# Performance work log

Measured on AMD Instinct MI355X. Metric: run time of the kernel, lower is better.

## Reference

```python
import jax, jax.numpy as jnp
import numpy as np

L, B, I, H, O = 8, 1, 2048, 2048, 1000  # num_layers, batch, input, hidden, output


def setup_inputs() -> dict:
    key = jax.random.key(0)
    ks = jax.random.split(key, 20)
    s = 1.0 / np.sqrt(H)  # torch nn.Linear default init bound

    def w(k, shape):
        return jax.random.uniform(k, shape, jnp.float32, -s, s)

    inp = {
        "x": jax.random.normal(ks[0], (B, 1, I), jnp.float32),
        "h": jax.random.normal(ks[1], (L, B, H), jnp.float32),
    }
    # six gate linears per layer; input_size == hidden_size so all stack to [L, H, H]
    for i, n in enumerate(["W_ir", "W_hr", "W_h1", "W_x1", "W_iu", "W_hu"]):
        inp[n] = w(ks[2 + 2 * i], (L, H, H))
        inp["b" + n[1:]] = w(ks[3 + 2 * i], (L, H))
    inp["W_fc"] = w(ks[14], (O, H))
    inp["b_fc"] = w(ks[15], (O,))
    return inp


def reference(x, h, W_ir, b_ir, W_hr, b_hr, W_h1, b_h1, W_x1, b_x1,
              W_iu, b_iu, W_hu, b_hu, W_fc, b_fc):
    # Layer 0 input is x[:, 0, :]; layer l>0 input is the ORIGINAL h[l-1]
    # (not the freshly computed hidden), so all layers are independent -> batch them.
    inp = jnp.concatenate([x[:, 0, :][None, :, :], h[:-1]], axis=0)  # [L, B, H]

    def lin(v, W, b):  # per-layer torch Linear: v @ W.T + b, batched over L
        return jnp.einsum('lbi,lhi->lbh', v, W) + b[:, None, :]

    reset_gate = jax.nn.sigmoid(lin(inp, W_ir, b_ir) + lin(h, W_hr, b_hr))
    r = jnp.tanh(reset_gate * lin(h, W_h1, b_h1) + lin(inp, W_x1, b_x1))
    update_gate = jax.nn.sigmoid(lin(inp, W_iu, b_iu) + lin(h, W_hu, b_hu))
    new_h = (1.0 - update_gate) * r + update_gate * h  # [L, B, H]

    out = jax.nn.log_softmax(jnp.maximum(new_h[-1], 0.0) @ W_fc.T + b_fc, axis=1)
    return (out, new_h)
```

## Files before the change

### kernel.cpp

```cpp
#include <hip/hip_runtime.h>
#include <math.h>

#define NL 8
#define NH 2048
#define NO 1000

__device__ __forceinline__ float dot4(float4 a, float4 b) {
    return a.x * b.x + a.y * b.y + a.z * b.z + a.w * b.w;
}

__device__ __forceinline__ float4 relu4(float4 a) {
    return make_float4(fmaxf(a.x, 0.f), fmaxf(a.y, 0.f), fmaxf(a.z, 0.f), fmaxf(a.w, 0.f));
}

__device__ __forceinline__ float wave_sum(float v) {
#pragma unroll
    for (int off = 32; off > 0; off >>= 1) v += __shfl_xor(v, off);
    return v;
}

__global__ __launch_bounds__(384) void gru_gates_kernel(
    const float* __restrict__ x,
    const float* __restrict__ h,
    const float* __restrict__ W_ir, const float* __restrict__ b_ir,
    const float* __restrict__ W_hr, const float* __restrict__ b_hr,
    const float* __restrict__ W_h1, const float* __restrict__ b_h1,
    const float* __restrict__ W_x1, const float* __restrict__ b_x1,
    const float* __restrict__ W_iu, const float* __restrict__ b_iu,
    const float* __restrict__ W_hu, const float* __restrict__ b_hu,
    float* __restrict__ new_h)
{
    const int bi   = blockIdx.x;
    const int l    = bi >> 11;
    const int g    = threadIdx.x >> 6;
    const int lane = threadIdx.x & 63;

    __shared__ float part[6];

    const float* __restrict__ W;
    const float* __restrict__ bv;
    const float* vecf;
    const float* vi = (l == 0) ? x : (h + (size_t)(l - 1) * NH);
    const float* vh = h + (size_t)l * NH;
    switch (g) {
        case 0:  W = W_ir; bv = b_ir; vecf = vi; break;
        case 1:  W = W_hr; bv = b_hr; vecf = vh; break;
        case 2:  W = W_h1; bv = b_h1; vecf = vh; break;
        case 3:  W = W_x1; bv = b_x1; vecf = vi; break;
        case 4:  W = W_iu; bv = b_iu; vecf = vi; break;
        default: W = W_hu; bv = b_hu; vecf = vh; break;
    }
    const float4* __restrict__ wrow = (const float4*)(W + (size_t)bi * NH);
    const float4* __restrict__ vec  = (const float4*)vecf;

    const float4 w0 = wrow[lane +   0];
    const float4 w1 = wrow[lane +  64];
    const float4 w2 = wrow[lane + 128];
    const float4 w3 = wrow[lane + 192];
    const float4 w4 = wrow[lane + 256];
    const float4 w5 = wrow[lane + 320];
    const float4 w6 = wrow[lane + 384];
    const float4 w7 = wrow[lane + 448];

    float s;
    s  = dot4(vec[lane +   0], w0);
    s += dot4(vec[lane +  64], w1);
    s += dot4(vec[lane + 128], w2);
    s += dot4(vec[lane + 192], w3);
    s += dot4(vec[lane + 256], w4);
    s += dot4(vec[lane + 320], w5);
    s += dot4(vec[lane + 384], w6);
    s += dot4(vec[lane + 448], w7);

    s = wave_sum(s);
    if (lane == 0) part[g] = s + bv[bi];
    __syncthreads();

    if (threadIdx.x == 0) {
        const float reset = 1.f / (1.f + expf(-(part[0] + part[1])));
        const float r     = tanhf(reset * part[2] + part[3]);
        const float u     = 1.f / (1.f + expf(-(part[4] + part[5])));
        const float hv    = h[bi];
        new_h[bi] = (1.f - u) * r + u * hv;
    }
}

__global__ __launch_bounds__(256) void fc_kernel(
    const float* __restrict__ new_h,
    const float* __restrict__ W_fc,
    const float* __restrict__ b_fc,
    float* __restrict__ logits)
{
    const int wave = (blockIdx.x * blockDim.x + threadIdx.x) >> 6;
    const int lane = threadIdx.x & 63;
    if (wave >= NO) return;
    const float4* __restrict__ v = (const float4*)(new_h + (size_t)(NL - 1) * NH);
    const float4* __restrict__ w = (const float4*)(W_fc + (size_t)wave * NH);
    float s = 0.f;
#pragma unroll
    for (int it = 0; it < NH / 4 / 64 / 2; ++it) {
        const int k0 = it * 128 + lane;
        const int k1 = k0 + 64;
        const float4 v0 = v[k0];
        const float4 w0 = w[k0];
        const float4 v1 = v[k1];
        const float4 w1 = w[k1];
        s += dot4(relu4(v0), w0) + dot4(relu4(v1), w1);
    }
    s = wave_sum(s);
    if (lane == 0) logits[wave] = s + b_fc[wave];
}

__global__ __launch_bounds__(1024) void lsm_kernel(
    const float* __restrict__ logits, float* __restrict__ out)
{
    const int t = threadIdx.x;
    const int lane = t & 63;
    const int wid = t >> 6;
    __shared__ float sred[16];

    const float v = (t < NO) ? logits[t] : -INFINITY;

    float m = v;
#pragma unroll
    for (int off = 32; off > 0; off >>= 1) m = fmaxf(m, __shfl_xor(m, off));
    if (lane == 0) sred[wid] = m;
    __syncthreads();
    if (wid == 0) {
        float mm = (t < 16) ? sred[t] : -INFINITY;
#pragma unroll
        for (int off = 8; off > 0; off >>= 1) mm = fmaxf(mm, __shfl_xor(mm, off));
        if (t == 0) sred[0] = mm;
    }
    __syncthreads();
    const float M = sred[0];
    __syncthreads();

    float e = (t < NO) ? expf(v - M) : 0.f;
    float s = e;
#pragma unroll
    for (int off = 32; off > 0; off >>= 1) s += __shfl_xor(s, off);
    if (lane == 0) sred[wid] = s;
    __syncthreads();
    if (wid == 0) {
        float ss = (t < 16) ? sred[t] : 0.f;
#pragma unroll
        for (int off = 8; off > 0; off >>= 1) ss += __shfl_xor(ss, off);
        if (t == 0) sred[0] = ss;
    }
    __syncthreads();
    const float lse = M + logf(sred[0]);

    if (t < NO) out[t] = v - lse;
}

extern "C" void kernel_launch(void* const* d_in, const int* in_sizes, int n_in,
                              void* d_out, int out_size, void* d_ws, size_t ws_size,
                              hipStream_t stream) {
    const float* x    = (const float*)d_in[0];
    const float* h    = (const float*)d_in[1];
    const float* W_ir = (const float*)d_in[2];
    const float* b_ir = (const float*)d_in[3];
    const float* W_hr = (const float*)d_in[4];
    const float* b_hr = (const float*)d_in[5];
    const float* W_h1 = (const float*)d_in[6];
    const float* b_h1 = (const float*)d_in[7];
    const float* W_x1 = (const float*)d_in[8];
    const float* b_x1 = (const float*)d_in[9];
    const float* W_iu = (const float*)d_in[10];
    const float* b_iu = (const float*)d_in[11];
    const float* W_hu = (const float*)d_in[12];
    const float* b_hu = (const float*)d_in[13];
    const float* W_fc = (const float*)d_in[14];
    const float* b_fc = (const float*)d_in[15];

    float* out    = (float*)d_out;
    float* new_h  = out + NO;
    float* logits = (float*)d_ws;

    gru_gates_kernel<<<NL * NH, 384, 0, stream>>>(
        x, h, W_ir, b_ir, W_hr, b_hr, W_h1, b_h1, W_x1, b_x1,
        W_iu, b_iu, W_hu, b_hu, new_h);

    fc_kernel<<<(NO + 3) / 4, 256, 0, stream>>>(new_h, W_fc, b_fc, logits);

    lsm_kernel<<<1, 1024, 0, stream>>>(logits, out);
}
```

Before: 141.4 us.

## Process four rows per GRU block and fuse FC with log-softmax via last-block counter

The gate kernel now has each block handle four consecutive output rows, so each wave loads its input vector once and reuses it across four weight rows. This cuts the block count fourfold and amortizes vector loads and the block-level sync. The FC and log-softmax kernels are merged: a global atomic counter picks the last finishing block, which then computes the log-softmax over all logits, removing one kernel launch. The price is an extra memset launch, per-block atomics and fences, and higher register pressure in the gate kernel.

```diff
diff --git a/kernel.cpp b/kernel.cpp
--- a/kernel.cpp
+++ b/kernel.cpp
@@ -4,13 +4,10 @@
 #define NL 8
 #define NH 2048
 #define NO 1000
+#define ROWS 4
 
 __device__ __forceinline__ float dot4(float4 a, float4 b) {
     return a.x * b.x + a.y * b.y + a.z * b.z + a.w * b.w;
-}
-
-__device__ __forceinline__ float4 relu4(float4 a) {
-    return make_float4(fmaxf(a.x, 0.f), fmaxf(a.y, 0.f), fmaxf(a.z, 0.f), fmaxf(a.w, 0.f));
 }
 
 __device__ __forceinline__ float wave_sum(float v) {
@@ -30,18 +27,18 @@
     const float* __restrict__ W_hu, const float* __restrict__ b_hu,
     float* __restrict__ new_h)
 {
-    const int bi   = blockIdx.x;
-    const int l    = bi >> 11;
+    const int row0 = blockIdx.x * ROWS;
+    const int l    = row0 >> 11;
     const int g    = threadIdx.x >> 6;
     const int lane = threadIdx.x & 63;
 
-    __shared__ float part[6];
-
+    __shared__ float part[ROWS][6];
+
+    const float* vi = (l == 0) ? x : (h + (size_t)(l - 1) * NH);
+    const float* vh = h + (size_t)l * NH;
     const float* __restrict__ W;
     const float* __restrict__ bv;
     const float* vecf;
-    const float* vi = (l == 0) ? x : (h + (size_t)(l - 1) * NH);
-    const float* vh = h + (size_t)l * NH;
     switch (g) {
         case 0:  W = W_ir; bv = b_ir; vecf = vi; break;
         case 1:  W = W_hr; bv = b_hr; vecf = vh; break;
@@ -50,108 +47,147 @@
         case 4:  W = W_iu; bv = b_iu; vecf = vi; break;
         default: W = W_hu; bv = b_hu; vecf = vh; break;
     }
-    const float4* __restrict__ wrow = (const float4*)(W + (size_t)bi * NH);
-    const float4* __restrict__ vec  = (const float4*)vecf;
-
-    const float4 w0 = wrow[lane +   0];
-    const float4 w1 = wrow[lane +  64];
-    const float4 w2 = wrow[lane + 128];
-    const float4 w3 = wrow[lane + 192];
-    const float4 w4 = wrow[lane + 256];
-    const float4 w5 = wrow[lane + 320];
-    const float4 w6 = wrow[lane + 384];
-    const float4 w7 = wrow[lane + 448];
-
-    float s;
-    s  = dot4(vec[lane +   0], w0);
-    s += dot4(vec[lane +  64], w1);
-    s += dot4(vec[lane + 128], w2);
-    s += dot4(vec[lane + 192], w3);
-    s += dot4(vec[lane + 256], w4);
-    s += dot4(vec[lane + 320], w5);
-    s += dot4(vec[lane + 384], w6);
-    s += dot4(vec[lane + 448], w7);
-
-    s = wave_sum(s);
-    if (lane == 0) part[g] = s + bv[bi];
-    __syncthreads();
-
-    if (threadIdx.x == 0) {
-        const float reset = 1.f / (1.f + expf(-(part[0] + part[1])));
-        const float r     = tanhf(reset * part[2] + part[3]);
-        const float u     = 1.f / (1.f + expf(-(part[4] + part[5])));
-        const float hv    = h[bi];
-        new_h[bi] = (1.f - u) * r + u * hv;
-    }
-}
-
-__global__ __launch_bounds__(256) void fc_kernel(
+    const float4* __restrict__ vec = (const float4*)vecf;
+
+    const float4 v0 = vec[lane +   0];
+    const float4 v1 = vec[lane +  64];
+    const float4 v2 = vec[lane + 128];
+    const float4 v3 = vec[lane + 192];
+    const float4 v4 = vec[lane + 256];
+    const float4 v5 = vec[lane + 320];
+    const float4 v6 = vec[lane + 384];
+    const float4 v7 = vec[lane + 448];
+
+    const float4* __restrict__ wrow = (const float4*)(W + (size_t)row0 * NH);
+
+    float s0, s1, s2, s3;
+    {
+        const float4* __restrict__ wr = wrow;
+        const float4 w0 = wr[lane +   0], w1 = wr[lane +  64];
+        const float4 w2 = wr[lane + 128], w3 = wr[lane + 192];
+        const float4 w4 = wr[lane + 256], w5 = wr[lane + 320];
+        const float4 w6 = wr[lane + 384], w7 = wr[lane + 448];
+        s0 = dot4(v0,w0)+dot4(v1,w1)+dot4(v2,w2)+dot4(v3,w3)
+           + dot4(v4,w4)+dot4(v5,w5)+dot4(v6,w6)+dot4(v7,w7);
+    }
+    {
+        const float4* __restrict__ wr = wrow + (NH / 4);
+        const float4 w0 = wr[lane +   0], w1 = wr[lane +  64];
+        const float4 w2 = wr[lane + 128], w3 = wr[lane + 192];
+        const float4 w4 = wr[lane + 256], w5 = wr[lane + 320];
+        const float4 w6 = wr[lane + 384], w7 = wr[lane + 448];
+        s1 = dot4(v0,w0)+dot4(v1,w1)+dot4(v2,w2)+dot4(v3,w3)
+           + dot4(v4,w4)+dot4(v5,w5)+dot4(v6,w6)+dot4(v7,w7);
+    }
+    {
+        const float4* __restrict__ wr = wrow + 2 * (NH / 4);
+        const float4 w0 = wr[lane +   0], w1 = wr[lane +  64];
+        const float4 w2 = wr[lane + 128], w3 = wr[lane + 192];
+        const float4 w4 = wr[lane + 256], w5 = wr[lane + 320];
+        const float4 w6 = wr[lane + 384], w7 = wr[lane + 448];
+        s2 = dot4(v0,w0)+dot4(v1,w1)+dot4(v2,w2)+dot4(v3,w3)
+           + dot4(v4,w4)+dot4(v5,w5)+dot4(v6,w6)+dot4(v7,w7);
+    }
+    {
+        const float4* __restrict__ wr = wrow + 3 * (NH / 4);
+        const float4 w0 = wr[lane +   0], w1 = wr[lane +  64];
+        const float4 w2 = wr[lane + 128], w3 = wr[lane + 192];
+        const float4 w4 = wr[lane + 256], w5 = wr[lane + 320];
+        const float4 w6 = wr[lane + 384], w7 = wr[lane + 448];
+        s3 = dot4(v0,w0)+dot4(v1,w1)+dot4(v2,w2)+dot4(v3,w3)
+           + dot4(v4,w4)+dot4(v5,w5)+dot4(v6,w6)+dot4(v7,w7);
+    }
+
+    s0 = wave_sum(s0);
+    s1 = wave_sum(s1);
+    s2 = wave_sum(s2);
+    s3 = wave_sum(s3);
+    if (lane == 0) {
+        part[0][g] = s0 + bv[row0 + 0];
+        part[1][g] = s1 + bv[row0 + 1];
+        part[2][g] = s2 + bv[row0 + 2];
+        part[3][g] = s3 + bv[row0 + 3];
+    }
+    __syncthreads();
+
+    if (threadIdx.x < ROWS) {
+        const int r  = threadIdx.x;
+        const int bi = row0 + r;
+        const float reset = 1.f / (1.f + expf(-(part[r][0] + part[r][1])));
+        const float rr    = tanhf(reset * part[r][2] + part[r][3]);
+        const float u     = 1.f / (1.f + expf(-(part[r][4] + part[r][5])));
+        new_h[bi] = (1.f - u) * rr + u * h[bi];
+    }
+}
+
+__global__ __launch_bounds__(256) void fc_lsm_kernel(
     const float* __restrict__ new_h,
     const float* __restrict__ W_fc,
     const float* __restrict__ b_fc,
-    float* __restrict__ logits)
+    float* __restrict__ logits,
+    unsigned int* __restrict__ counter,
+    float* __restrict__ out)
 {
-    const int wave = (blockIdx.x * blockDim.x + threadIdx.x) >> 6;
     const int lane = threadIdx.x & 63;
-    if (wave >= NO) return;
-    const float4* __restrict__ v = (const float4*)(new_h + (size_t)(NL - 1) * NH);
-    const float4* __restrict__ w = (const float4*)(W_fc + (size_t)wave * NH);
-    float s = 0.f;
-#pragma unroll
-    for (int it = 0; it < NH / 4 / 64 / 2; ++it) {
-        const int k0 = it * 128 + lane;
-        const int k1 = k0 + 64;
-        const float4 v0 = v[k0];
-        const float4 w0 = w[k0];
-        const float4 v1 = v[k1];
-        const float4 w1 = w[k1];
-        s += dot4(relu4(v0), w0) + dot4(relu4(v1), w1);
-    }
-    s = wave_sum(s);
-    if (lane == 0) logits[wave] = s + b_fc[wave];
-}
-
-__global__ __launch_bounds__(1024) void lsm_kernel(
-    const float* __restrict__ logits, float* __restrict__ out)
-{
+    const int wid  = threadIdx.x >> 6;
+    const int row  = blockIdx.x * 4 + wid;
+
+    if (row < NO) {
+        const float4* __restrict__ v  = (const float4*)(new_h + (size_t)(NL - 1) * NH);
+        const float4* __restrict__ wt = (const float4*)(W_fc + (size_t)row * NH);
+        float s = 0.f;
+#pragma unroll
+        for (int c = 0; c < 8; ++c) {
+            const int k = c * 64 + lane;
+            float4 vv = v[k];
+            vv.x = fmaxf(vv.x, 0.f); vv.y = fmaxf(vv.y, 0.f);
+            vv.z = fmaxf(vv.z, 0.f); vv.w = fmaxf(vv.w, 0.f);
+            s += dot4(vv, wt[k]);
+        }
+        s = wave_sum(s);
+        if (lane == 0) logits[row] = s + b_fc[row];
+    }
+    __threadfence();
+    __syncthreads();
+
+    __shared__ unsigned int lastflag;
+    if (threadIdx.x == 0)
+        lastflag = (atomicAdd(counter, 1u) == gridDim.x - 1) ? 1u : 0u;
+    __syncthreads();
+    if (!lastflag) return;
+    __threadfence();
+
     const int t = threadIdx.x;
-    const int lane = t & 63;
-    const int wid = t >> 6;
-    __shared__ float sred[16];
-
-    const float v = (t < NO) ? logits[t] : -INFINITY;
-
-    float m = v;
+    float l0 = -INFINITY, l1 = -INFINITY, l2 = -INFINITY, l3 = -INFINITY;
+    if (t       < NO) l0 = logits[t];
+    if (t + 256 < NO) l1 = logits[t + 256];
+    if (t + 512 < NO) l2 = logits[t + 512];
+    if (t + 768 < NO) l3 = logits[t + 768];
+
+    __shared__ float redm[4];
+    float m = fmaxf(fmaxf(l0, l1), fmaxf(l2, l3));
 #pragma unroll
     for (int off = 32; off > 0; off >>= 1) m = fmaxf(m, __shfl_xor(m, off));
-    if (lane == 0) sred[wid] = m;
-    __syncthreads();
-    if (wid == 0) {
-        float mm = (t < 16) ? sred[t] : -INFINITY;
-#pragma unroll
-        for (int off = 8; off > 0; off >>= 1) mm = fmaxf(mm, __shfl_xor(mm, off));
-        if (t == 0) sred[0] = mm;
-    }
-    __syncthreads();
-    const float M = sred[0];
-    __syncthreads();
-
-    float e = (t < NO) ? expf(v - M) : 0.f;
-    float s = e;
-#pragma unroll
-    for (int off = 32; off > 0; off >>= 1) s += __shfl_xor(s, off);
-    if (lane == 0) sred[wid] = s;
-    __syncthreads();
-    if (wid == 0) {
-        float ss = (t < 16) ? sred[t] : 0.f;
-#pragma unroll
-        for (int off = 8; off > 0; off >>= 1) ss += __shfl_xor(ss, off);
-        if (t == 0) sred[0] = ss;
-    }
-    __syncthreads();
-    const float lse = M + logf(sred[0]);
-
-    if (t < NO) out[t] = v - lse;
+    if (lane == 0) redm[wid] = m;
+    __syncthreads();
+    m = fmaxf(fmaxf(redm[0], redm[1]), fmaxf(redm[2], redm[3]));
+
+    __shared__ float reds[4];
+    float e = 0.f;
+    if (t       < NO) e += expf(l0 - m);
+    if (t + 256 < NO) e += expf(l1 - m);
+    if (t + 512 < NO) e += expf(l2 - m);
+    if (t + 768 < NO) e += expf(l3 - m);
+#pragma unroll
+    for (int off = 32; off > 0; off >>= 1) e += __shfl_xor(e, off);
+    if (lane == 0) reds[wid] = e;
+    __syncthreads();
+    const float lse = m + logf(reds[0] + reds[1] + reds[2] + reds[3]);
+
+    if (t       < NO) out[t]       = l0 - lse;
+    if (t + 256 < NO) out[t + 256] = l1 - lse;
+    if (t + 512 < NO) out[t + 512] = l2 - lse;
+    if (t + 768 < NO) out[t + 768] = l3 - lse;
 }
 
 extern "C" void kernel_launch(void* const* d_in, const int* in_sizes, int n_in,
@@ -177,12 +213,14 @@
     float* out    = (float*)d_out;
     float* new_h  = out + NO;
     float* logits = (float*)d_ws;
-
-    gru_gates_kernel<<<NL * NH, 384, 0, stream>>>(
+    unsigned int* counter = (unsigned int*)((char*)d_ws + 4096);
+
+    hipMemsetAsync(counter, 0, sizeof(unsigned int), stream);
+
+    gru_gates_kernel<<<(NL * NH) / ROWS, 384, 0, stream>>>(
         x, h, W_ir, b_ir, W_hr, b_hr, W_h1, b_h1, W_x1, b_x1,
         W_iu, b_iu, W_hu, b_hu, new_h);
 
-    fc_kernel<<<(NO + 3) / 4, 256, 0, stream>>>(new_h, W_fc, b_fc, logits);
-
-    lsm_kernel<<<1, 1024, 0, stream>>>(logits, out);
-}
+    fc_lsm_kernel<<<(NO + 3) / 4, 256, 0, stream>>>(
+        new_h, W_fc, b_fc, logits, counter, out);
+}
```

Result: slower. 164.6 us (+16.4%).
